# Performance work log

Measured on AMD Instinct MI355X. Metric: run time of the kernel, lower is better.

Reference implementation:

```python
import jax, jax.numpy as jnp
import numpy as np

B = 4096          # batch == in_features (required by the module's broadcast)
F = 4096          # in_features
OUT = 4096        # out_features


def _pairwise_l2(x):
    # torch.cdist(x, x, p=2): exact pairwise Euclidean distances [B, B]
    sq = jnp.sum(x * x, axis=-1)                       # [B]
    d2 = sq[:, None] + sq[None, :] - 2.0 * (x @ x.T)   # [B, B]
    d2 = jnp.maximum(d2, 0.0)
    # safe sqrt: zero distance (diagonal) -> 0 with zero subgradient
    d = jnp.sqrt(jnp.where(d2 > 0.0, d2, 1.0))
    return jnp.where(d2 > 0.0, d, 0.0)


def setup_inputs() -> dict:
    key = jax.random.key(0)
    k1, k2, k3, k4 = jax.random.split(key, 4)
    x = jax.random.normal(k1, (B, F), dtype=jnp.float32)
    # nn.Linear default init: U(-1/sqrt(fan_in), 1/sqrt(fan_in))
    lim_rbf = 1.0 / np.sqrt(F)
    lim_out = 1.0 / np.sqrt(F)
    W_rbf = jax.random.uniform(k2, (F, F), minval=-lim_rbf, maxval=lim_rbf, dtype=jnp.float32)
    W_out = jax.random.uniform(k3, (OUT, F), minval=-lim_out, maxval=lim_out, dtype=jnp.float32)
    b_out = jax.random.uniform(k4, (OUT,), minval=-lim_out, maxval=lim_out, dtype=jnp.float32)
    return {"x": x, "W_rbf": W_rbf, "W_out": W_out, "b_out": b_out}


def reference(x, W_rbf, W_out, b_out):
    dist = _pairwise_l2(x)                    # [B, B]
    gram = jnp.exp(-jnp.abs(W_rbf) * dist)    # [B, B] (B == F so broadcast is elementwise)
    mixed = gram @ x                          # [B, F]
    return mixed @ W_out.T + b_out            # [B, OUT]
```

## Files before the change

### kernel.cpp

```cpp
#include <hip/hip_runtime.h>
#include <cstdint>

#define LDD 4096
#define NT 64

typedef __attribute__((ext_vector_type(8))) short short8;
typedef __attribute__((ext_vector_type(4))) float f32x4;

__device__ __forceinline__ short f2bf(float f) {
  uint32_t u = __builtin_bit_cast(uint32_t, f);
  u += 0x7fffu + ((u >> 16) & 1u);
  return (short)(u >> 16);
}

__device__ __forceinline__ void async16(const void* g, void* l) {
  __builtin_amdgcn_global_load_lds(
      (const __attribute__((address_space(1))) unsigned*)(uintptr_t)g,
      (__attribute__((address_space(3))) unsigned*)(uintptr_t)l,
      16, 0, 0);
}

__global__ __launch_bounds__(256)
void prep_rows(const float* __restrict__ x, short* __restrict__ xb,
               float* __restrict__ sq) {
  int row = blockIdx.x, tid = threadIdx.x;
  const float4* xr = (const float4*)(x + (size_t)row * LDD);
  short4* xo = (short4*)(xb + (size_t)row * LDD);
  float s = 0.f;
#pragma unroll
  for (int i = 0; i < 4; i++) {
    float4 v = xr[i * 256 + tid];
    s = fmaf(v.x, v.x, s); s = fmaf(v.y, v.y, s);
    s = fmaf(v.z, v.z, s); s = fmaf(v.w, v.w, s);
    short4 o; o.x = f2bf(v.x); o.y = f2bf(v.y); o.z = f2bf(v.z); o.w = f2bf(v.w);
    xo[i * 256 + tid] = o;
  }
#pragma unroll
  for (int off = 32; off > 0; off >>= 1) s += __shfl_down(s, off, 64);
  __shared__ float red[4];
  int lane = tid & 63, wv = tid >> 6;
  if (lane == 0) red[wv] = s;
  __syncthreads();
  if (tid == 0) sq[row] = red[0] + red[1] + red[2] + red[3];
}

__global__ __launch_bounds__(256)
void transpose_bf16(const float* __restrict__ x, short* __restrict__ xT) {
  __shared__ float tile[64][65];
  int bx = blockIdx.x, by = blockIdx.y, tid = threadIdx.x;
  int tr = tid >> 4;
  int tc = (tid & 15) << 2;
#pragma unroll
  for (int i = 0; i < 4; i++) {
    int r = i * 16 + tr;
    float4 v = *(const float4*)(x + (size_t)(by * 64 + r) * LDD + bx * 64 + tc);
    tile[r][tc + 0] = v.x; tile[r][tc + 1] = v.y;
    tile[r][tc + 2] = v.z; tile[r][tc + 3] = v.w;
  }
  __syncthreads();
#pragma unroll
  for (int i = 0; i < 4; i++) {
    int fr = i * 16 + tr;
    short4 o;
    o.x = f2bf(tile[tc + 0][fr]); o.y = f2bf(tile[tc + 1][fr]);
    o.z = f2bf(tile[tc + 2][fr]); o.w = f2bf(tile[tc + 3][fr]);
    *(short4*)(xT + (size_t)(bx * 64 + fr) * LDD + by * 64 + tc) = o;
  }
}

__global__ __launch_bounds__(256)
void conv_bf16(const float* __restrict__ w, short* __restrict__ wb) {
  int i = blockIdx.x * 256 + threadIdx.x;
  float4 v = ((const float4*)w)[i];
  short4 o; o.x = f2bf(v.x); o.y = f2bf(v.y); o.z = f2bf(v.z); o.w = f2bf(v.w);
  ((short4*)wb)[i] = o;
}

template <int MODE>
__global__ __launch_bounds__(512, 2)
void gemm256(const short* __restrict__ A, const short* __restrict__ Bt,
             short* __restrict__ outB, float* __restrict__ outF,
             const float* __restrict__ extra, const float* __restrict__ sq) {
  __shared__ __attribute__((aligned(16))) char smem[131072];
  const int tid = threadIdx.x;

  int bid = blockIdx.x;
  int lin = (bid & 7) * 32 + (bid >> 3);
  const int rb = (lin >> 4) * 256;
  const int cb = (lin & 15) * 256;

  const int s0 = tid, s1 = 512 + tid;
  const int r0 = s0 >> 3, c0 = (s0 & 7) ^ (r0 & 7);
  const int r1 = s1 >> 3, c1 = (s1 & 7) ^ (r1 & 7);
  const size_t go0 = (size_t)r0 * LDD + (size_t)(c0 << 3);
  const size_t go1 = (size_t)r1 * LDD + (size_t)(c1 << 3);

  const short* gB0 = Bt + (size_t)cb * LDD;
  const short* gB1 = Bt + (size_t)(cb + 128) * LDD;
  const short* gA0 = A + (size_t)rb * LDD;
  const short* gA1 = A + (size_t)(rb + 128) * LDD;
  char* lst = smem + tid * 16;

  auto stage = [&](const short* g, int tt, int half) {
    const short* gp = g + (size_t)tt * 64;
    char* l = lst + ((tt & 1) << 16) + (half << 14);
    async16(gp + go0, l);
    async16(gp + go1, l + 8192);
  };

  const int lane = tid & 63;
  const int wv = tid >> 6;
  const int wm = wv >> 2;
  const int wn = wv & 3;
  const int fr = lane & 15;
  const int fq = lane >> 4;
  const int arow = fr * 128;
  const int brow = ((wn & 1) * 64 + fr) * 128;
  const int sx0 = ((fq ^ (fr & 7)) << 4);
  const int sx1 = (((4 + fq) ^ (fr & 7)) << 4);
  const int abase = 32768 + (wm << 14);
  const int bbase = (wn >> 1) << 14;

  f32x4 acc[8][4];
#pragma unroll
  for (int m = 0; m < 8; ++m)
#pragma unroll
    for (int n = 0; n < 4; ++n) acc[m][n] = {0.f, 0.f, 0.f, 0.f};

  stage(gB0, 0, 0); stage(gB1, 0, 1); stage(gA0, 0, 2); stage(gA1, 0, 3);
  stage(gB0, 1, 0); stage(gB1, 1, 1);
  asm volatile("s_waitcnt vmcnt(4)" ::: "memory");
  __builtin_amdgcn_s_barrier();

  short8 av[4][2], bv[4][2];

  for (int t = 0; t < NT; ++t) {
    const int bufo = (t & 1) << 16;
    const char* ab = smem + bufo + abase;
    const char* bb = smem + bufo + bbase;

#pragma unroll
    for (int n = 0; n < 4; ++n) {
      bv[n][0] = *(const short8*)(bb + brow + n * 2048 + sx0);
      bv[n][1] = *(const short8*)(bb + brow + n * 2048 + sx1);
    }
#pragma unroll
    for (int m = 0; m < 4; ++m) {
      av[m][0] = *(const short8*)(ab + arow + m * 2048 + sx0);
      av[m][1] = *(const short8*)(ab + arow + m * 2048 + sx1);
    }
    if (t + 1 < NT) stage(gA0, t + 1, 2);
    __builtin_amdgcn_s_barrier();
    asm volatile("s_waitcnt lgkmcnt(0)" ::: "memory");
    __builtin_amdgcn_s_setprio(1);
#pragma unroll
    for (int m = 0; m < 4; ++m)
#pragma unroll
      for (int n = 0; n < 2; ++n)
#pragma unroll
        for (int kk = 0; kk < 2; ++kk)
          acc[m][n] = __builtin_amdgcn_mfma_f32_16x16x32_bf16(
              av[m][kk], bv[n][kk], acc[m][n], 0, 0, 0);
    __builtin_amdgcn_s_setprio(0);
    __builtin_amdgcn_s_barrier();

    if (t + 1 < NT) stage(gA1, t + 1, 3);
    __builtin_amdgcn_s_barrier();
    __builtin_amdgcn_s_setprio(1);
#pragma unroll
    for (int m = 0; m < 4; ++m)
#pragma unroll
      for (int n = 2; n < 4; ++n)
#pragma unroll
        for (int kk = 0; kk < 2; ++kk)
          acc[m][n] = __builtin_amdgcn_mfma_f32_16x16x32_bf16(
              av[m][kk], bv[n][kk], acc[m][n], 0, 0, 0);
    __builtin_amdgcn_s_setprio(0);
    __builtin_amdgcn_s_barrier();

#pragma unroll
    for (int m = 0; m < 4; ++m) {
      av[m][0] = *(const short8*)(ab + 8192 + arow + m * 2048 + sx0);
      av[m][1] = *(const short8*)(ab + 8192 + arow + m * 2048 + sx1);
    }
    if (t + 2 < NT) stage(gB0, t + 2, 0);
    __builtin_amdgcn_s_barrier();
    asm volatile("s_waitcnt lgkmcnt(0)" ::: "memory");
    __builtin_amdgcn_s_setprio(1);
#pragma unroll
    for (int m = 0; m < 4; ++m)
#pragma unroll
      for (int n = 0; n < 2; ++n)
#pragma unroll
        for (int kk = 0; kk < 2; ++kk)
          acc[4 + m][n] = __builtin_amdgcn_mfma_f32_16x16x32_bf16(
              av[m][kk], bv[n][kk], acc[4 + m][n], 0, 0, 0);
    __builtin_amdgcn_s_setprio(0);
    __builtin_amdgcn_s_barrier();

    if (t + 2 < NT) stage(gB1, t + 2, 1);
    __builtin_amdgcn_s_barrier();
    __builtin_amdgcn_s_setprio(1);
#pragma unroll
    for (int m = 0; m < 4; ++m)
#pragma unroll
      for (int n = 2; n < 4; ++n)
#pragma unroll
        for (int kk = 0; kk < 2; ++kk)
          acc[4 + m][n] = __builtin_amdgcn_mfma_f32_16x16x32_bf16(
              av[m][kk], bv[n][kk], acc[4 + m][n], 0, 0, 0);
    __builtin_amdgcn_s_setprio(0);
    if (t + 2 < NT) asm volatile("s_waitcnt vmcnt(4)" ::: "memory");
    else            asm volatile("s_waitcnt vmcnt(0)" ::: "memory");
    __builtin_amdgcn_s_barrier();
  }

  const int orow = rb + wm * 128 + fq * 4;
  const int ocol = cb + wn * 64 + fr;
  if (MODE == 0) {
    float sqc[4];
#pragma unroll
    for (int n = 0; n < 4; ++n) sqc[n] = sq[ocol + n * 16];
#pragma unroll
    for (int m = 0; m < 8; ++m) {
#pragma unroll
      for (int rr = 0; rr < 4; ++rr) {
        int row = orow + m * 16 + rr;
        float sqr = sq[row];
#pragma unroll
        for (int n = 0; n < 4; ++n) {
          size_t idx = (size_t)row * LDD + ocol + n * 16;
          float d2 = sqr + sqc[n] - 2.0f * acc[m][n][rr];
          float d = sqrtf(fmaxf(d2, 0.f));
          outB[idx] = f2bf(__expf(-fabsf(extra[idx]) * d));
        }
      }
    }
  } else if (MODE == 1) {
#pragma unroll
    for (int m = 0; m < 8; ++m)
#pragma unroll
      for (int rr = 0; rr < 4; ++rr) {
        int row = orow + m * 16 + rr;
#pragma unroll
        for (int n = 0; n < 4; ++n)
          outB[(size_t)row * LDD + ocol + n * 16] = f2bf(acc[m][n][rr]);
      }
  } else {
    float bc[4];
#pragma unroll
    for (int n = 0; n < 4; ++n) bc[n] = extra[ocol + n * 16];
#pragma unroll
    for (int m = 0; m < 8; ++m)
#pragma unroll
      for (int rr = 0; rr < 4; ++rr) {
        int row = orow + m * 16 + rr;
#pragma unroll
        for (int n = 0; n < 4; ++n)
          outF[(size_t)row * LDD + ocol + n * 16] = acc[m][n][rr] + bc[n];
      }
  }
}

extern "C" void kernel_launch(void* const* d_in, const int* in_sizes, int n_in,
                              void* d_out, int out_size, void* d_ws, size_t ws_size,
                              hipStream_t stream) {
  const float* x    = (const float*)d_in[0];
  const float* Wrbf = (const float*)d_in[1];
  const float* Wout = (const float*)d_in[2];
  const float* bout = (const float*)d_in[3];
  float* out = (float*)d_out;

  char* ws = (char*)d_ws;
  short* xb    = (short*)ws;
  float* sq    = (float*)(ws + (size_t)32 * 1024 * 1024);
  short* woutb = (short*)(ws + (size_t)32 * 1024 * 1024);
  short* gram  = (short*)d_out;
  short* xT    = (short*)((char*)d_out + (size_t)32 * 1024 * 1024);
  short* mixed = xb;

  prep_rows<<<LDD, 256, 0, stream>>>(x, xb, sq);
  transpose_bf16<<<dim3(64, 64), 256, 0, stream>>>(x, xT);
  gemm256<0><<<256, 512, 0, stream>>>(xb, xb, gram, nullptr, Wrbf, sq);
  gemm256<1><<<256, 512, 0, stream>>>(gram, xT, mixed, nullptr, nullptr, nullptr);
  conv_bf16<<<LDD * LDD / 4 / 256, 256, 0, stream>>>(Wout, woutb);
  gemm256<2><<<256, 512, 0, stream>>>(mixed, woutb, nullptr, out, bout, nullptr);
}
```

Baseline: 561.3 us.

## Software-pipeline A-fragment LDS reads with MFMA and cut per-iteration barriers

Restructures the GEMM main loop to split the A fragments into two ping-pong register sets (avX/avY) so LDS reads for the next 2-row chunk are issued while MFMAs on the current chunk run. Waits use partial lgkmcnt counts instead of full drains. The first A chunk of the next tile is prefetched after the end-of-iteration barrier. The loop drops from about eight barriers per iteration to two, and sched_barrier fences pin the instruction order. This aims to hide LDS latency and barrier stalls, at the cost of relying on careful ordering to avoid races on the shared buffers.

After: 517.4 us. 1.08x faster.

```diff
diff --git a/kernel.cpp b/kernel.cpp
--- a/kernel.cpp
+++ b/kernel.cpp
@@ -75,6 +75,9 @@
   short4 o; o.x = f2bf(v.x); o.y = f2bf(v.y); o.z = f2bf(v.z); o.w = f2bf(v.w);
   ((short4*)wb)[i] = o;
 }
+
+#define SB() __builtin_amdgcn_sched_barrier(0)
+#define LGKM(n) do { asm volatile("s_waitcnt lgkmcnt(" #n ")" ::: "memory"); SB(); } while (0)
 
 template <int MODE>
 __global__ __launch_bounds__(512, 2)
@@ -127,92 +130,76 @@
 #pragma unroll
     for (int n = 0; n < 4; ++n) acc[m][n] = {0.f, 0.f, 0.f, 0.f};
 
+#define RD_AV(dst, base_off, ap)                                        \
+  do {                                                                  \
+    dst[0][0] = *(const short8*)((ap) + (base_off) + arow + sx0);       \
+    dst[0][1] = *(const short8*)((ap) + (base_off) + arow + sx1);       \
+    dst[1][0] = *(const short8*)((ap) + (base_off) + 2048 + arow + sx0);\
+    dst[1][1] = *(const short8*)((ap) + (base_off) + 2048 + arow + sx1);\
+  } while (0)
+
+#define MM(av2, mb)                                                     \
+  do {                                                                  \
+    __builtin_amdgcn_s_setprio(1);                                      \
+    _Pragma("unroll")                                                   \
+    for (int kk = 0; kk < 2; ++kk)                                      \
+      _Pragma("unroll")                                                 \
+      for (int mi = 0; mi < 2; ++mi)                                    \
+        _Pragma("unroll")                                               \
+        for (int n = 0; n < 4; ++n)                                     \
+          acc[(mb) + mi][n] = __builtin_amdgcn_mfma_f32_16x16x32_bf16(  \
+              av2[mi][kk], bv[n][kk], acc[(mb) + mi][n], 0, 0, 0);      \
+    __builtin_amdgcn_s_setprio(0);                                      \
+  } while (0)
+
+  short8 avX[2][2], avY[2][2], bv[4][2];
+
   stage(gB0, 0, 0); stage(gB1, 0, 1); stage(gA0, 0, 2); stage(gA1, 0, 3);
   stage(gB0, 1, 0); stage(gB1, 1, 1);
   asm volatile("s_waitcnt vmcnt(4)" ::: "memory");
   __builtin_amdgcn_s_barrier();
-
-  short8 av[4][2], bv[4][2];
+  RD_AV(avX, 0, smem + abase);
+  SB();
 
   for (int t = 0; t < NT; ++t) {
     const int bufo = (t & 1) << 16;
     const char* ab = smem + bufo + abase;
     const char* bb = smem + bufo + bbase;
+    const char* abn = smem + (bufo ^ (1 << 16)) + abase;
 
 #pragma unroll
     for (int n = 0; n < 4; ++n) {
       bv[n][0] = *(const short8*)(bb + brow + n * 2048 + sx0);
       bv[n][1] = *(const short8*)(bb + brow + n * 2048 + sx1);
     }
-#pragma unroll
-    for (int m = 0; m < 4; ++m) {
-      av[m][0] = *(const short8*)(ab + arow + m * 2048 + sx0);
-      av[m][1] = *(const short8*)(ab + arow + m * 2048 + sx1);
-    }
+    SB();
+    RD_AV(avY, 4096, ab);
+    SB();
     if (t + 1 < NT) stage(gA0, t + 1, 2);
+    LGKM(4);
     __builtin_amdgcn_s_barrier();
-    asm volatile("s_waitcnt lgkmcnt(0)" ::: "memory");
-    __builtin_amdgcn_s_setprio(1);
-#pragma unroll
-    for (int m = 0; m < 4; ++m)
-#pragma unroll
-      for (int n = 0; n < 2; ++n)
-#pragma unroll
-        for (int kk = 0; kk < 2; ++kk)
-          acc[m][n] = __builtin_amdgcn_mfma_f32_16x16x32_bf16(
-              av[m][kk], bv[n][kk], acc[m][n], 0, 0, 0);
-    __builtin_amdgcn_s_setprio(0);
-    __builtin_amdgcn_s_barrier();
-
+    MM(avX, 0);
+
+    RD_AV(avX, 8192, ab);
+    SB();
     if (t + 1 < NT) stage(gA1, t + 1, 3);
-    __builtin_amdgcn_s_barrier();
-    __builtin_amdgcn_s_setprio(1);
-#pragma unroll
-    for (int m = 0; m < 4; ++m)
-#pragma unroll
-      for (int n = 2; n < 4; ++n)
-#pragma unroll
-        for (int kk = 0; kk < 2; ++kk)
-          acc[m][n] = __builtin_amdgcn_mfma_f32_16x16x32_bf16(
-              av[m][kk], bv[n][kk], acc[m][n], 0, 0, 0);
-    __builtin_amdgcn_s_setprio(0);
-    __builtin_amdgcn_s_barrier();
-
-#pragma unroll
-    for (int m = 0; m < 4; ++m) {
-      av[m][0] = *(const short8*)(ab + 8192 + arow + m * 2048 + sx0);
-      av[m][1] = *(const short8*)(ab + 8192 + arow + m * 2048 + sx1);
-    }
+    LGKM(4);
+    MM(avY, 2);
+
+    RD_AV(avY, 8192 + 4096, ab);
+    SB();
     if (t + 2 < NT) stage(gB0, t + 2, 0);
-    __builtin_amdgcn_s_barrier();
-    asm volatile("s_waitcnt lgkmcnt(0)" ::: "memory");
-    __builtin_amdgcn_s_setprio(1);
-#pragma unroll
-    for (int m = 0; m < 4; ++m)
-#pragma unroll
-      for (int n = 0; n < 2; ++n)
-#pragma unroll
-        for (int kk = 0; kk < 2; ++kk)
-          acc[4 + m][n] = __builtin_amdgcn_mfma_f32_16x16x32_bf16(
-              av[m][kk], bv[n][kk], acc[4 + m][n], 0, 0, 0);
-    __builtin_amdgcn_s_setprio(0);
-    __builtin_amdgcn_s_barrier();
+    LGKM(4);
+    MM(avX, 4);
 
     if (t + 2 < NT) stage(gB1, t + 2, 1);
-    __builtin_amdgcn_s_barrier();
-    __builtin_amdgcn_s_setprio(1);
-#pragma unroll
-    for (int m = 0; m < 4; ++m)
-#pragma unroll
-      for (int n = 2; n < 4; ++n)
-#pragma unroll
-        for (int kk = 0; kk < 2; ++kk)
-          acc[4 + m][n] = __builtin_amdgcn_mfma_f32_16x16x32_bf16(
-              av[m][kk], bv[n][kk], acc[4 + m][n], 0, 0, 0);
-    __builtin_amdgcn_s_setprio(0);
+    LGKM(0);
     if (t + 2 < NT) asm volatile("s_waitcnt vmcnt(4)" ::: "memory");
     else            asm volatile("s_waitcnt vmcnt(0)" ::: "memory");
     __builtin_amdgcn_s_barrier();
+    if (t + 1 < NT) { RD_AV(avX, 0, abn); }
+    SB();
+    MM(avY, 6);
   }
 
   const int orow = rb + wm * 128 + fq * 4;
@@ -260,6 +247,8 @@
           outF[(size_t)row * LDD + ocol + n * 16] = acc[m][n][rr] + bc[n];
       }
   }
+#undef RD_AV
+#undef MM
 }
 
 extern "C" void kernel_launch(void* const* d_in, const int* in_sizes, int n_in,
```
